# Kernel optimization log

Hardware: AMD Instinct MI355X
Metric: run time of the kernel (lower is better)

The kernel has to match this reference:

```python
import jax, jax.numpy as jnp
import numpy as np

EPS = 1e-5
NEG_SLOPE = 0.2

def _bn(x, g, b, m, v):
    # eval-mode BatchNorm over channel axis 1
    sh = (1, -1) + (1,) * (x.ndim - 2)
    inv = g.reshape(sh) * jax.lax.rsqrt(v.reshape(sh) + EPS)
    return (x - m.reshape(sh)) * inv + b.reshape(sh)

def _lrelu(x):
    return jnp.where(x >= 0, x, NEG_SLOPE * x)

def _edge_feature(x, idx):
    # x: [B,C,N], idx: [B,N,k] -> edge diffs [B,C,N,k]
    xT = jnp.transpose(x, (0, 2, 1))                      # [B,N,C]
    B = x.shape[0]
    neigh = xT[jnp.arange(B)[:, None, None], idx]         # [B,N,k,C]
    e = neigh - xT[:, :, None, :]                         # [B,N,k,C]
    return jnp.transpose(e, (0, 3, 1, 2))                 # [B,C,N,k]

def _edgeconv(x, idx, w, g, b, m, v):
    e = _edge_feature(x, idx)                             # [B,Cin,N,k]
    y = jnp.einsum('bcnk,oc->bonk', e, w)                 # 1x1 conv2d, no bias
    y = _lrelu(_bn(y, g, b, m, v))
    return jnp.max(y, axis=-1)                            # max over k -> [B,Cout,N]

def _pointconv(x, w, g, b, m, v):
    y = jnp.einsum('bcn,oc->bon', x, w)                   # 1x1 conv1d, no bias
    return _lrelu(_bn(y, g, b, m, v))

def setup_inputs() -> dict:
    key = jax.random.key(0)
    B, N, K = 8, 4096, 20
    ks = jax.random.split(key, 40)
    it = iter(range(40))
    d = {}
    d['x'] = jax.random.normal(ks[next(it)], (B, 3, N), dtype=jnp.float32)
    d['idx'] = jax.random.randint(ks[next(it)], (B, N, K), 0, N, dtype=jnp.int32)
    dims = [(64, 3), (64, 64), (128, 64), (256, 128), (256, 512), (128, 256), (1, 128)]
    for i, (o, c) in enumerate(dims, 1):
        d[f'w{i}'] = jax.random.normal(ks[next(it)], (o, c), dtype=jnp.float32) * (1.0 / np.sqrt(c))
    for i, c in enumerate([64, 64, 128, 256, 256, 128], 1):
        d[f'g{i}'] = jax.random.uniform(ks[next(it)], (c,), dtype=jnp.float32, minval=0.5, maxval=1.5)
        d[f'b{i}'] = jax.random.normal(ks[next(it)], (c,), dtype=jnp.float32) * 0.1
        d[f'm{i}'] = jax.random.normal(ks[next(it)], (c,), dtype=jnp.float32) * 0.1
        d[f'v{i}'] = jax.random.uniform(ks[next(it)], (c,), dtype=jnp.float32, minval=0.5, maxval=1.5)
    return d

def reference(x, idx, w1, w2, w3, w4, w5, w6, w7,
              g1, b1, m1, v1, g2, b2, m2, v2, g3, b3, m3, v3,
              g4, b4, m4, v4, g5, b5, m5, v5, g6, b6, m6, v6):
    x1 = _edgeconv(x,  idx, w1, g1, b1, m1, v1)   # [B,64,N]
    x2 = _edgeconv(x1, idx, w2, g2, b2, m2, v2)   # [B,64,N]
    x3 = _edgeconv(x2, idx, w3, g3, b3, m3, v3)   # [B,128,N]
    x4 = _edgeconv(x3, idx, w4, g4, b4, m4, v4)   # [B,256,N]
    h = jnp.concatenate((x1, x2, x3, x4), axis=1) # [B,512,N]
    h = _pointconv(h, w5, g5, b5, m5, v5)         # [B,256,N]
    h = _pointconv(h, w6, g6, b6, m6, v6)         # [B,128,N]
    h = _lrelu(jnp.einsum('bcn,oc->bon', h, w7))  # [B,1,N]
    return jnp.transpose(h, (0, 2, 1))            # [B,N,1]
```

## Files before the change

### kernel.cpp

```cpp
#include <hip/hip_runtime.h>
#include <hip/hip_bf16.h>
#include <cstdint>
#include <cstddef>

#define EPS 1e-5f
#define NEG 0.2f

static constexpr int B_ = 8, N_ = 4096, K_ = 20, M_ = B_ * N_;

typedef __attribute__((ext_vector_type(8))) _Float16 f16x8;
typedef __attribute__((ext_vector_type(4))) float f32x4;

__device__ __forceinline__ void gload_lds16(const _Float16* g, _Float16* l) {
  __builtin_amdgcn_global_load_lds(
      (const __attribute__((address_space(1))) uint32_t*)g,
      (__attribute__((address_space(3))) uint32_t*)l, 16, 0, 0);
}

__global__ __launch_bounds__(256) void prep_c3(
    const float* __restrict__ x, const float* __restrict__ w1,
    const float* __restrict__ w2, const float* __restrict__ w3,
    const float* __restrict__ w4, const float* __restrict__ w5,
    const float* __restrict__ w6,
    const float* __restrict__ g1, const float* __restrict__ b1, const float* __restrict__ m1, const float* __restrict__ v1,
    const float* __restrict__ g2, const float* __restrict__ b2, const float* __restrict__ m2, const float* __restrict__ v2,
    const float* __restrict__ g3, const float* __restrict__ b3, const float* __restrict__ m3, const float* __restrict__ v3,
    const float* __restrict__ g4, const float* __restrict__ b4, const float* __restrict__ m4, const float* __restrict__ v4,
    const float* __restrict__ g5, const float* __restrict__ b5, const float* __restrict__ m5, const float* __restrict__ v5,
    const float* __restrict__ g6, const float* __restrict__ b6, const float* __restrict__ m6, const float* __restrict__ v6,
    float* __restrict__ P, _Float16* __restrict__ Wh, _Float16* __restrict__ z) {
  const int bid = blockIdx.x, tid = threadIdx.x;
  if (bid < 512) {
    const int o  = tid & 63;
    const int pi = tid >> 6;
    const float ww0 = w1[o * 3 + 0], ww1 = w1[o * 3 + 1], ww2 = w1[o * 3 + 2];
    const float iv = g1[o] * rsqrtf(v1[o] + EPS);
    const int pbase = bid * 64;
    const int b = pbase >> 12;
    const int nbase = pbase & (N_ - 1);
    const float* xb = x + (size_t)b * 3 * N_;
    for (int pj = pi; pj < 64; pj += 4) {
      const int n = nbase + pj;
      const float x0 = xb[n], x1v = xb[N_ + n], x2v = xb[2 * N_ + n];
      z[(size_t)(pbase + pj) * 64 + o] = (_Float16)((x0 * ww0 + x1v * ww1 + x2v * ww2) * iv);
    }
    return;
  }
  if (bid == 1328) {
    const float* G[6]  = {g1, g2, g3, g4, g5, g6};
    const float* Bb[6] = {b1, b2, b3, b4, b5, b6};
    const float* Mm[6] = {m1, m2, m3, m4, m5, m6};
    const float* Vv[6] = {v1, v2, v3, v4, v5, v6};
    const int Cs[6] = {64, 64, 128, 256, 256, 128};
    const int OI[6] = {0, 128, 256, 512, 1024, 1536};
    const int OB[6] = {64, 192, 384, 768, 1280, 1664};
    for (int l = 0; l < 6; ++l) {
      for (int c = tid; c < Cs[l]; c += 256) {
        float iv = G[l][c] * rsqrtf(Vv[l][c] + EPS);
        P[OI[l] + c] = iv;
        P[OB[l] + c] = Bb[l][c] - Mm[l][c] * iv;
      }
    }
    return;
  }
  const int fb = bid - 512;
  const float* w; const float* g; const float* v; _Float16* dst; int lc, base;
  if (fb < 16)       { w = w2; g = g2; v = v2; dst = Wh + 0;      lc = 6; base = 0;   }
  else if (fb < 48)  { w = w3; g = g3; v = v3; dst = Wh + 4096;   lc = 6; base = 16;  }
  else if (fb < 176) { w = w4; g = g4; v = v4; dst = Wh + 12288;  lc = 7; base = 48;  }
  else if (fb < 688) { w = w5; g = g5; v = v5; dst = Wh + 45056;  lc = 9; base = 176; }
  else               { w = w6; g = g6; v = v6; dst = Wh + 176128; lc = 8; base = 688; }
  const int e = (fb - base) * 256 + tid;
  const int o = e >> lc;
  dst[e] = (_Float16)(w[e] * (g[o] * rsqrtf(v[o] + EPS)));
}

template <int BO>
__global__ __launch_bounds__(256) void edge_gemm64(
    const _Float16* __restrict__ z, const int* __restrict__ idx,
    const float* __restrict__ betap,
    const _Float16* __restrict__ W,
    _Float16* __restrict__ hout,
    _Float16* __restrict__ zout, int ldzout) {
  constexpr int GW = BO / 8;
  constexpr int OJ = BO / 32;
  __shared__ _Float16 Asmem[128 * 64];
  __shared__ _Float16 Wsmem[BO * 64];

  const int tid = threadIdx.x, lane = tid & 63, wid = tid >> 6;
  const int batch = blockIdx.x & 7, chunk = blockIdx.x >> 3;
  const int bm0 = (batch << 12) + chunk * 128;
  const int lr = lane & 15, lk = lane >> 4;

  const _Float16* Wbase = W + (size_t)lr * 64 + lk * 8;
#pragma unroll
  for (int g = wid; g < GW; g += 4) {
    const int o = g >> 1, s = g & 1;
    gload_lds16(Wbase + (size_t)16 * o * 64 + s * 32, Wsmem + g * 512);
  }

  const int lid = tid & 7, cb = lid * 8;
  float bt[8];
#pragma unroll
  for (int q = 0; q < 8; ++q) bt[q] = betap[cb + q];
  const _Float16* zb = z + ((size_t)(batch << 12)) * 64;
#pragma unroll
  for (int pass = 0; pass < 4; ++pass) {
    const int pi = pass * 32 + (tid >> 3);
    const int p = bm0 + pi;
    const int* ip = idx + (size_t)p * K_;
    const int ir0 = ip[lid];
    const int ir1 = ip[8 + lid];
    const int ir2 = ip[16 + (lid & 3)];
    f16x8 mx = *reinterpret_cast<const f16x8*>(zb + (size_t)__shfl(ir0, 0, 8) * 64 + cb);
#pragma unroll
    for (int k = 1; k < K_; ++k) {
      const int g = (k < 8) ? __shfl(ir0, k, 8)
                  : (k < 16) ? __shfl(ir1, k - 8, 8)
                             : __shfl(ir2, k - 16, 8);
      const f16x8 v = *reinterpret_cast<const f16x8*>(zb + (size_t)g * 64 + cb);
#pragma unroll
      for (int q = 0; q < 8; ++q) mx[q] = v[q] > mx[q] ? v[q] : mx[q];
    }
    const f16x8 vc = *reinterpret_cast<const f16x8*>(z + (size_t)p * 64 + cb);
    f16x8 vo;
#pragma unroll
    for (int q = 0; q < 8; ++q) {
      const float e = (float)mx[q] - (float)vc[q] + bt[q];
      vo[q] = (_Float16)fmaxf(e, NEG * e);
    }
    *reinterpret_cast<f16x8*>(hout + (size_t)p * 512 + cb) = vo;
    const int i = pi >> 4, rr = pi & 15, s = cb >> 5, kk = (cb >> 3) & 3;
    *reinterpret_cast<f16x8*>(Asmem + (i * 2 + s) * 512 + ((kk << 4) | rr) * 8) = vo;
  }
  __syncthreads();

  const int wr = wid >> 1, wc = wid & 1;
  f32x4 acc[4][OJ];
#pragma unroll
  for (int i = 0; i < 4; ++i)
#pragma unroll
    for (int j = 0; j < OJ; ++j) acc[i][j] = (f32x4){0.f, 0.f, 0.f, 0.f};
#pragma unroll
  for (int s = 0; s < 2; ++s) {
    f16x8 av[4], wv[OJ];
#pragma unroll
    for (int i = 0; i < 4; ++i)
      av[i] = *reinterpret_cast<const f16x8*>(Asmem + ((wr * 4 + i) * 2 + s) * 512 + lane * 8);
#pragma unroll
    for (int j = 0; j < OJ; ++j)
      wv[j] = *reinterpret_cast<const f16x8*>(Wsmem + ((wc * OJ + j) * 2 + s) * 512 + lane * 8);
#pragma unroll
    for (int i = 0; i < 4; ++i)
#pragma unroll
      for (int j = 0; j < OJ; ++j)
        acc[i][j] = __builtin_amdgcn_mfma_f32_16x16x32_f16(av[i], wv[j], acc[i][j], 0, 0, 0);
  }

#pragma unroll
  for (int j = 0; j < OJ; ++j) {
    const int o = wc * (BO / 2) + 16 * j + lr;
#pragma unroll
    for (int i = 0; i < 4; ++i) {
      const int r0 = bm0 + wr * 64 + 16 * i + lk * 4;
#pragma unroll
      for (int q = 0; q < 4; ++q)
        zout[(size_t)(r0 + q) * ldzout + o] = (_Float16)acc[i][j][q];
    }
  }
}

template <int BM, int BO, int C, int MODE>
__global__ __launch_bounds__(256) void gemm_pipe(
    const _Float16* __restrict__ A, int lda,
    const _Float16* __restrict__ W,
    const float* __restrict__ betap,
    _Float16* __restrict__ out, int ldout,
    const float* __restrict__ w7, float* __restrict__ dout) {
  constexpr int NK = C / 32;
  constexpr int GA = BM / 16;
  constexpr int GW = BO / 16;
  constexpr int GT = GA + GW;
  constexpr int GP = GT / 4;
  constexpr int SB = (BM + BO) * 32;
  constexpr int MI = BM / 32, OJ = BO / 32;
  __shared__ _Float16 lds[4 * SB];

  const int lane = threadIdx.x & 63;
  const int wid  = threadIdx.x >> 6;
  const int wr = wid >> 1, wc = wid & 1;
  const int bm0 = blockIdx.x * BM;
  const int bo0 = blockIdx.y * BO;
  const int lr = lane & 15, lk = lane >> 4;

  const _Float16* Abase = A + (size_t)(bm0 + lr) * lda + lk * 8;
  const _Float16* Wbase = W + (size_t)(bo0 + lr) * C + lk * 8;

  f32x4 acc[MI][OJ];
#pragma unroll
  for (int i = 0; i < MI; ++i)
#pragma unroll
    for (int j = 0; j < OJ; ++j) acc[i][j] = (f32x4){0.f, 0.f, 0.f, 0.f};

  auto stage = [&](int buf, int k0) {
    _Float16* dst = &lds[buf * SB];
#pragma unroll
    for (int q = 0; q < GP; ++q) {
      const int g = wid * GP + q;
      const _Float16* src = (g < GA)
          ? Abase + (size_t)16 * g * lda + k0
          : Wbase + (size_t)16 * (g - GA) * C + k0;
      gload_lds16(src, dst + g * 512);
    }
  };

  auto compute = [&](int buf) {
    const _Float16* Ab = &lds[buf * SB];
    const _Float16* Wb = &lds[buf * SB + GA * 512];
    f16x8 av[MI], wv[OJ];
#pragma unroll
    for (int i = 0; i < MI; ++i)
      av[i] = *reinterpret_cast<const f16x8*>(Ab + (wr * MI + i) * 512 + lane * 8);
#pragma unroll
    for (int j = 0; j < OJ; ++j)
      wv[j] = *reinterpret_cast<const f16x8*>(Wb + (wc * OJ + j) * 512 + lane * 8);
#pragma unroll
    for (int i = 0; i < MI; ++i)
#pragma unroll
      for (int j = 0; j < OJ; ++j)
        acc[i][j] = __builtin_amdgcn_mfma_f32_16x16x32_f16(av[i], wv[j], acc[i][j], 0, 0, 0);
  };

  stage(0, 0);
  stage(1, 32);
#pragma unroll
  for (int t = 0; t < NK; ++t) {
    if (t + 2 < NK) {
      stage((t + 2) & 3, (t + 2) * 32);
      if constexpr (GP == 4) asm volatile("s_waitcnt vmcnt(8)" ::: "memory");
      else                   asm volatile("s_waitcnt vmcnt(6)" ::: "memory");
    } else if (t + 1 < NK) {
      if constexpr (GP == 4) asm volatile("s_waitcnt vmcnt(4)" ::: "memory");
      else                   asm volatile("s_waitcnt vmcnt(3)" ::: "memory");
    } else {
      asm volatile("s_waitcnt vmcnt(0)" ::: "memory");
    }
    __builtin_amdgcn_s_barrier();
    compute(t & 3);
  }

  if constexpr (MODE == 2) {
    __shared__ float dotbuf[BM][2];
    float rowdot[MI][4];
#pragma unroll
    for (int i = 0; i < MI; ++i)
#pragma unroll
      for (int q = 0; q < 4; ++q) rowdot[i][q] = 0.f;
#pragma unroll
    for (int j = 0; j < OJ; ++j) {
      const int o = wc * (BO / 2) + 16 * j + lr;
      const float bt = betap[o];
      const float wf = w7[o];
#pragma unroll
      for (int i = 0; i < MI; ++i)
#pragma unroll
        for (int q = 0; q < 4; ++q) {
          float t = acc[i][j][q] + bt;
          t = fmaxf(t, NEG * t);
          rowdot[i][q] += t * wf;
        }
    }
#pragma unroll
    for (int i = 0; i < MI; ++i)
#pragma unroll
      for (int q = 0; q < 4; ++q) {
#pragma unroll
        for (int off = 1; off < 16; off <<= 1)
          rowdot[i][q] += __shfl_xor(rowdot[i][q], off, 16);
        if (lr == 0) dotbuf[wr * (BM / 2) + 16 * i + lk * 4 + q][wc] = rowdot[i][q];
      }
    __syncthreads();
    if (threadIdx.x < BM) {
      const float s = dotbuf[threadIdx.x][0] + dotbuf[threadIdx.x][1];
      dout[bm0 + threadIdx.x] = fmaxf(s, NEG * s);
    }
    return;
  }

#pragma unroll
  for (int j = 0; j < OJ; ++j) {
    const int o = bo0 + wc * (BO / 2) + 16 * j + lr;
    const float bt = (MODE == 1) ? betap[o] : 0.f;
#pragma unroll
    for (int i = 0; i < MI; ++i) {
      const int r0 = bm0 + wr * (BM / 2) + 16 * i + lk * 4;
#pragma unroll
      for (int q = 0; q < 4; ++q) {
        float t = acc[i][j][q];
        if (MODE == 1) { t += bt; t = fmaxf(t, NEG * t); }
        out[(size_t)(r0 + q) * ldout + o] = (_Float16)t;
      }
    }
  }
}

template <int O>
__global__ __launch_bounds__(256) void edge_max8(
    const _Float16* __restrict__ z, const int* __restrict__ idx,
    const float* __restrict__ betap, _Float16* __restrict__ out, int ldout) {
  constexpr int TPP = O / 8;
  constexpr int PPB = 256 / TPP;
  constexpr int NW = (K_ + TPP - 1) / TPP;
  const int t = threadIdx.x;
  const int batch = blockIdx.x & 7;
  const int chunk = blockIdx.x >> 3;
  const int p = (batch << 12) + chunk * PPB + t / TPP;
  const int lid = t % TPP;
  const int cb = lid * 8;
  const int* ip = idx + (size_t)p * K_;
  int ir[NW];
#pragma unroll
  for (int wv = 0; wv < NW; ++wv) {
    const int l = wv * TPP + lid;
    ir[wv] = (l < K_) ? ip[l] : ip[0];
  }
  const _Float16* zb = z + ((size_t)(batch << 12)) * O;

  f16x8 mx = *reinterpret_cast<const f16x8*>(zb + (size_t)__shfl(ir[0], 0, TPP) * O + cb);
#pragma unroll
  for (int k = 1; k < K_; ++k) {
    const int g = __shfl(ir[k / TPP], k % TPP, TPP);
    const f16x8 v = *reinterpret_cast<const f16x8*>(zb + (size_t)g * O + cb);
#pragma unroll
    for (int q = 0; q < 8; ++q) mx[q] = v[q] > mx[q] ? v[q] : mx[q];
  }
  const f16x8 vc = *reinterpret_cast<const f16x8*>(z + (size_t)p * O + cb);
  f16x8 vo;
#pragma unroll
  for (int q = 0; q < 8; ++q) {
    const float e = (float)mx[q] - (float)vc[q] + betap[cb + q];
    vo[q] = (_Float16)fmaxf(e, NEG * e);
  }
  *reinterpret_cast<f16x8*>(out + (size_t)p * ldout + cb) = vo;
}

extern "C" void kernel_launch(void* const* d_in, const int* in_sizes, int n_in,
                              void* d_out, int out_size, void* d_ws, size_t ws_size,
                              hipStream_t stream) {
  const float* x  = (const float*)d_in[0];
  const int* idx  = (const int*)d_in[1];
  const float* w[7];
  for (int i = 0; i < 7; ++i) w[i] = (const float*)d_in[2 + i];
  const float* bn[24];
  for (int i = 0; i < 24; ++i) bn[i] = (const float*)d_in[9 + i];

  float* P       = (float*)d_ws;
  _Float16* Wh   = (_Float16*)((char*)d_ws + (32 << 10));
  _Float16* z_a  = (_Float16*)((char*)d_ws + (1u << 20));
  _Float16* h512 = (_Float16*)((char*)d_ws + (17u << 20));
  _Float16* z_b  = (_Float16*)((char*)d_ws + (49u << 20));

  prep_c3<<<1329, 256, 0, stream>>>(
      x, w[0], w[1], w[2], w[3], w[4], w[5],
      bn[0], bn[1], bn[2], bn[3],   bn[4], bn[5], bn[6], bn[7],
      bn[8], bn[9], bn[10], bn[11], bn[12], bn[13], bn[14], bn[15],
      bn[16], bn[17], bn[18], bn[19], bn[20], bn[21], bn[22], bn[23],
      P, Wh, z_a);

  const float* bt1 = P + 64;
  const float* bt2 = P + 192;
  const float* bt3 = P + 384;
  const float* bt4 = P + 768;
  const float* bt5 = P + 1280;
  const float* bt6 = P + 1664;
  const _Float16* W2 = Wh + 0, *W3 = Wh + 4096, *W4 = Wh + 12288,
               *W5 = Wh + 45056, *W6 = Wh + 176128;

  edge_gemm64<64><<<M_ / 128, 256, 0, stream>>>(z_a, idx, bt1, W2, h512 + 0, z_b, 64);
  edge_gemm64<128><<<M_ / 128, 256, 0, stream>>>(z_b, idx, bt2, W3, h512 + 64, z_a, 128);
  edge_max8<128><<<M_ / 16, 256, 0, stream>>>(z_a, idx, bt3, h512 + 128, 512);
  gemm_pipe<128, 128, 128, 0><<<dim3(M_ / 128, 2), 256, 0, stream>>>(
      h512 + 128, 512, W4, nullptr, z_b, 256, nullptr, nullptr);
  edge_max8<256><<<M_ / 8, 256, 0, stream>>>(z_b, idx, bt4, h512 + 256, 512);
  gemm_pipe<128, 128, 512, 1><<<dim3(M_ / 128, 2), 256, 0, stream>>>(
      h512, 512, W5, bt5, z_a, 256, nullptr, nullptr);
  gemm_pipe<64, 128, 256, 2><<<dim3(M_ / 64, 1), 256, 0, stream>>>(
      z_a, 256, W6, bt6, nullptr, 0, w[6], (float*)d_out);
}
```

Measured before the change: 102.4 us.

## Fuse layer-3 edge max with layer-4 GEMM and widen layer-5 GEMM tile

```diff
diff --git a/kernel.cpp b/kernel.cpp
--- a/kernel.cpp
+++ b/kernel.cpp
@@ -170,8 +170,98 @@
   }
 }
 
+__global__ __launch_bounds__(256, 1) void edge_gemm_full(
+    const _Float16* __restrict__ z, const int* __restrict__ idx,
+    const float* __restrict__ betap,
+    const _Float16* __restrict__ W,
+    _Float16* __restrict__ hout,
+    _Float16* __restrict__ zout) {
+  constexpr int CIN = 128, BO = 256;
+  __shared__ _Float16 Asmem[128 * CIN];
+  __shared__ _Float16 Wsmem[BO * CIN];
+
+  const int tid = threadIdx.x, lane = tid & 63, wid = tid >> 6;
+  const int batch = blockIdx.x & 7, chunk = blockIdx.x >> 3;
+  const int bm0 = (batch << 12) + chunk * 128;
+  const int lr = lane & 15, lk = lane >> 4;
+
+  const _Float16* Wbase = W + (size_t)lr * CIN + lk * 8;
+#pragma unroll
+  for (int g = wid; g < 64; g += 4) {
+    const int ob = g >> 2, kk = g & 3;
+    gload_lds16(Wbase + (size_t)16 * ob * CIN + kk * 32, Wsmem + g * 512);
+  }
+
+  const int lid = tid & 15, cb = lid * 8;
+  float bt[8];
+#pragma unroll
+  for (int q = 0; q < 8; ++q) bt[q] = betap[cb + q];
+  const _Float16* zb = z + ((size_t)(batch << 12)) * CIN;
+#pragma unroll
+  for (int pass = 0; pass < 8; ++pass) {
+    const int pi = pass * 16 + (tid >> 4);
+    const int p = bm0 + pi;
+    const int* ip = idx + (size_t)p * K_;
+    const int ir0 = ip[lid];
+    const int ir1 = ip[16 + (lid & 3)];
+    f16x8 mx = *reinterpret_cast<const f16x8*>(zb + (size_t)__shfl(ir0, 0, 16) * CIN + cb);
+#pragma unroll
+    for (int k = 1; k < K_; ++k) {
+      const int g = (k < 16) ? __shfl(ir0, k, 16) : __shfl(ir1, k - 16, 16);
+      const f16x8 v = *reinterpret_cast<const f16x8*>(zb + (size_t)g * CIN + cb);
+#pragma unroll
+      for (int q = 0; q < 8; ++q) mx[q] = v[q] > mx[q] ? v[q] : mx[q];
+    }
+    const f16x8 vc = *reinterpret_cast<const f16x8*>(z + (size_t)p * CIN + cb);
+    f16x8 vo;
+#pragma unroll
+    for (int q = 0; q < 8; ++q) {
+      const float e = (float)mx[q] - (float)vc[q] + bt[q];
+      vo[q] = (_Float16)fmaxf(e, NEG * e);
+    }
+    *reinterpret_cast<f16x8*>(hout + (size_t)p * 512 + cb) = vo;
+    *reinterpret_cast<f16x8*>(Asmem + ((pi >> 4) * 4 + (lid >> 2)) * 512 +
+                              (((lid & 3) << 4) | (pi & 15)) * 8) = vo;
+  }
+  __syncthreads();
+
+  const int wr = wid >> 1, wc = wid & 1;
+  f32x4 acc[4][8];
+#pragma unroll
+  for (int i = 0; i < 4; ++i)
+#pragma unroll
+    for (int j = 0; j < 8; ++j) acc[i][j] = (f32x4){0.f, 0.f, 0.f, 0.f};
+#pragma unroll
+  for (int kk = 0; kk < 4; ++kk) {
+    f16x8 av[4], wv[8];
+#pragma unroll
+    for (int i = 0; i < 4; ++i)
+      av[i] = *reinterpret_cast<const f16x8*>(Asmem + ((wr * 4 + i) * 4 + kk) * 512 + lane * 8);
+#pragma unroll
+    for (int j = 0; j < 8; ++j)
+      wv[j] = *reinterpret_cast<const f16x8*>(Wsmem + ((wc * 8 + j) * 4 + kk) * 512 + lane * 8);
+#pragma unroll
+    for (int i = 0; i < 4; ++i)
+#pragma unroll
+      for (int j = 0; j < 8; ++j)
+        acc[i][j] = __builtin_amdgcn_mfma_f32_16x16x32_f16(av[i], wv[j], acc[i][j], 0, 0, 0);
+  }
+
+#pragma unroll
+  for (int j = 0; j < 8; ++j) {
+    const int o = wc * 128 + 16 * j + lr;
+#pragma unroll
+    for (int i = 0; i < 4; ++i) {
+      const int r0 = bm0 + wr * 64 + 16 * i + lk * 4;
+#pragma unroll
+      for (int q = 0; q < 4; ++q)
+        zout[(size_t)(r0 + q) * 256 + o] = (_Float16)acc[i][j][q];
+    }
+  }
+}
+
 template <int BM, int BO, int C, int MODE>
-__global__ __launch_bounds__(256) void gemm_pipe(
+__global__ __launch_bounds__(256, 1) void gemm_pipe(
     const _Float16* __restrict__ A, int lda,
     const _Float16* __restrict__ W,
     const float* __restrict__ betap,
@@ -237,11 +327,13 @@
   for (int t = 0; t < NK; ++t) {
     if (t + 2 < NK) {
       stage((t + 2) & 3, (t + 2) * 32);
-      if constexpr (GP == 4) asm volatile("s_waitcnt vmcnt(8)" ::: "memory");
-      else                   asm volatile("s_waitcnt vmcnt(6)" ::: "memory");
+      if constexpr (GP == 3)      asm volatile("s_waitcnt vmcnt(6)" ::: "memory");
+      else if constexpr (GP == 4) asm volatile("s_waitcnt vmcnt(8)" ::: "memory");
+      else                        asm volatile("s_waitcnt vmcnt(12)" ::: "memory");
     } else if (t + 1 < NK) {
-      if constexpr (GP == 4) asm volatile("s_waitcnt vmcnt(4)" ::: "memory");
-      else                   asm volatile("s_waitcnt vmcnt(3)" ::: "memory");
+      if constexpr (GP == 3)      asm volatile("s_waitcnt vmcnt(3)" ::: "memory");
+      else if constexpr (GP == 4) asm volatile("s_waitcnt vmcnt(4)" ::: "memory");
+      else                        asm volatile("s_waitcnt vmcnt(6)" ::: "memory");
     } else {
       asm volatile("s_waitcnt vmcnt(0)" ::: "memory");
     }
@@ -290,14 +382,14 @@
 #pragma unroll
   for (int j = 0; j < OJ; ++j) {
     const int o = bo0 + wc * (BO / 2) + 16 * j + lr;
-    const float bt = (MODE == 1) ? betap[o] : 0.f;
+    const float bt = betap[o];
 #pragma unroll
     for (int i = 0; i < MI; ++i) {
       const int r0 = bm0 + wr * (BM / 2) + 16 * i + lk * 4;
 #pragma unroll
       for (int q = 0; q < 4; ++q) {
-        float t = acc[i][j][q];
-        if (MODE == 1) { t += bt; t = fmaxf(t, NEG * t); }
+        float t = acc[i][j][q] + bt;
+        t = fmaxf(t, NEG * t);
         out[(size_t)(r0 + q) * ldout + o] = (_Float16)t;
       }
     }
@@ -378,11 +470,9 @@
 
   edge_gemm64<64><<<M_ / 128, 256, 0, stream>>>(z_a, idx, bt1, W2, h512 + 0, z_b, 64);
   edge_gemm64<128><<<M_ / 128, 256, 0, stream>>>(z_b, idx, bt2, W3, h512 + 64, z_a, 128);
-  edge_max8<128><<<M_ / 16, 256, 0, stream>>>(z_a, idx, bt3, h512 + 128, 512);
-  gemm_pipe<128, 128, 128, 0><<<dim3(M_ / 128, 2), 256, 0, stream>>>(
-      h512 + 128, 512, W4, nullptr, z_b, 256, nullptr, nullptr);
+  edge_gemm_full<<<M_ / 128, 256, 0, stream>>>(z_a, idx, bt3, W4, h512 + 128, z_b);
   edge_max8<256><<<M_ / 8, 256, 0, stream>>>(z_b, idx, bt4, h512 + 256, 512);
-  gemm_pipe<128, 128, 512, 1><<<dim3(M_ / 128, 2), 256, 0, stream>>>(
+  gemm_pipe<128, 256, 512, 1><<<dim3(M_ / 128, 1), 256, 0, stream>>>(
       h512, 512, W5, bt5, z_a, 256, nullptr, nullptr);
   gemm_pipe<64, 128, 256, 2><<<dim3(M_ / 64, 1), 256, 0, stream>>>(
       z_a, 256, W6, bt6, nullptr, 0, w[6], (float*)d_out);
```

New measurement: 108.6 us. +6.0%, slower.
